# Kernel tuning notes

Measured on AMD Instinct MI355X. Metric: run time of the kernel, lower is better.

The kernel has to match this reference:

```python
import jax, jax.numpy as jnp
import numpy as np

LMAX, MMAX = 4, 2
L1 = LMAX + 1                      # 5 coefficients with m=0
NL = [LMAX + 1 - m for m in range(MMAX + 1)]   # [5,4,3] degrees per |m|
K = (LMAX + 1) ** 2                # 25 full SH coefficients
KR = NL[0] + 2 * sum(NL[1:])       # 19 coefficients with |m|<=mmax
# degree l of each row in the reduced (m-primary) layout:
# m=0: l=0..4 | m=+1: l=1..4 | m=-1: l=1..4 | m=+2: l=2..4 | m=-2: l=2..4
L_IDX = np.array([0,1,2,3,4, 1,2,3,4, 1,2,3,4, 2,3,4, 2,3,4])


def so2_conv(x, rad, w0, b0, wr1, wi1, wr2, wi2, c_out, extra):
    """SO(2)-equivariant conv over m-primary layout x: [E, KR, c_in].
    rad: optional per-edge radial weights [E, sum_m nl_m*c_in]."""
    E, _, c_in = x.shape
    # m = 0 block
    x0 = x[:, :L1].reshape(E, L1 * c_in)
    if rad is not None:
        x0 = x0 * rad[:, :L1 * c_in]
    y0 = x0 @ w0 + b0
    out0 = y0[:, :L1 * c_out].reshape(E, L1, c_out)
    gating = y0[:, L1 * c_out:] if extra else None
    outs = [out0]
    off_x, off_r = L1, L1 * c_in
    for nl, wr, wi in ((NL[1], wr1, wi1), (NL[2], wr2, wi2)):
        xr = x[:, off_x:off_x + nl].reshape(E, nl * c_in)
        xi = x[:, off_x + nl:off_x + 2 * nl].reshape(E, nl * c_in)
        if rad is not None:
            rm = rad[:, off_r:off_r + nl * c_in]
            xr, xi = xr * rm, xi * rm
        yr = xr @ wr - xi @ wi   # complex-style SO2 mixing
        yi = xi @ wr + xr @ wi
        outs += [yr.reshape(E, nl, c_out), yi.reshape(E, nl, c_out)]
        off_x += 2 * nl
        off_r += nl * c_in
    return jnp.concatenate(outs, axis=1), gating


def gate_act(gating, x):
    """GateActivation: silu on l=0 scalars, sigmoid gates per degree l>=1."""
    E, _, H = x.shape
    g = jax.nn.sigmoid(gating).reshape(E, LMAX, H)
    g_ext = jnp.concatenate([jnp.ones((E, 1, H), x.dtype), g], axis=1)
    out = x * g_ext[:, L_IDX]           # l=0 row gated by 1, replaced below
    return out.at[:, 0].set(jax.nn.silu(x[:, 0]))


def setup_inputs() -> dict:
    key = jax.random.key(0)
    ks = jax.random.split(key, 32)
    E, N, C, H, D, RH = 50000, 2500, 64, 64, 128, 64
    c_in1 = 2 * C
    rad_dim = sum(nl * c_in1 for nl in NL)          # 1536
    extra = LMAX * H                                 # 256

    def w(k, shape):
        return jax.random.normal(k, shape, jnp.float32) / np.sqrt(shape[0])

    inp = {
        'node_feats': jax.random.normal(ks[0], (N, K, C), jnp.float32),
        'edge_embeds': jax.random.normal(ks[1], (E, D), jnp.float32),
        'wigner': jax.random.normal(ks[2], (E, KR, K), jnp.float32) / np.sqrt(K),
        'wigner_inv': jax.random.normal(ks[3], (E, K, KR), jnp.float32) / np.sqrt(KR),
        'edge_envelope': jax.random.uniform(ks[4], (E, 1, 1), jnp.float32),
        'rad_w1': w(ks[5], (D, RH)), 'rad_b1': jnp.zeros((RH,), jnp.float32),
        'rad_w2': w(ks[6], (RH, rad_dim)), 'rad_b2': jnp.zeros((rad_dim,), jnp.float32),
        'w1_m0': w(ks[7], (L1 * c_in1, L1 * H + extra)),
        'b1_m0': jnp.zeros((L1 * H + extra,), jnp.float32),
        'w1_r1': w(ks[8], (NL[1] * c_in1, NL[1] * H)),
        'w1_i1': w(ks[9], (NL[1] * c_in1, NL[1] * H)),
        'w1_r2': w(ks[10], (NL[2] * c_in1, NL[2] * H)),
        'w1_i2': w(ks[11], (NL[2] * c_in1, NL[2] * H)),
        'w2_m0': w(ks[12], (L1 * H, L1 * C)),
        'b2_m0': jnp.zeros((L1 * C,), jnp.float32),
        'w2_r1': w(ks[13], (NL[1] * H, NL[1] * C)),
        'w2_i1': w(ks[14], (NL[1] * H, NL[1] * C)),
        'w2_r2': w(ks[15], (NL[2] * H, NL[2] * C)),
        'w2_i2': w(ks[16], (NL[2] * H, NL[2] * C)),
        'senders': jax.random.randint(ks[17], (E,), 0, N, jnp.int32),
        'receivers': jax.random.randint(ks[18], (E,), 0, N, jnp.int32),
    }
    return inp


def reference(node_feats, edge_embeds, wigner, wigner_inv, edge_envelope,
              rad_w1, rad_b1, rad_w2, rad_b2,
              w1_m0, b1_m0, w1_r1, w1_i1, w1_r2, w1_i2,
              w2_m0, b2_m0, w2_r1, w2_i1, w2_r2, w2_i2,
              senders, receivers):
    num_nodes = node_feats.shape[0]
    C = node_feats.shape[2]
    H = w2_m0.shape[0] // L1
    # gather + concat: [E, K, 2C]
    msg = jnp.concatenate((node_feats[senders], node_feats[receivers]), axis=2)
    # rotate to edge frame, truncated to |m|<=mmax: [E, KR, 2C]
    msg = jnp.einsum('erk,ekc->erc', wigner, msg)
    # per-edge radial weights for conv1
    rad = jax.nn.silu(edge_embeds @ rad_w1 + rad_b1) @ rad_w2 + rad_b2
    msg, gating = so2_conv(msg, rad, w1_m0, b1_m0, w1_r1, w1_i1, w1_r2, w1_i2,
                           c_out=H, extra=LMAX * H)
    msg = gate_act(gating, msg)
    msg, _ = so2_conv(msg, None, w2_m0, b2_m0, w2_r1, w2_i1, w2_r2, w2_i2,
                      c_out=C, extra=0)
    msg = msg * edge_envelope
    # rotate back to global frame: [E, K, C]
    msg = jnp.einsum('ekr,erc->ekc', wigner_inv, msg)
    return jax.ops.segment_sum(msg, receivers, num_segments=num_nodes)
```

## Files before the change

kernel.cpp:

```cpp
#include <hip/hip_runtime.h>


typedef __attribute__((ext_vector_type(8))) short bf16x8;
typedef __attribute__((ext_vector_type(4))) float f32x4;

union U8 { uint4 v; unsigned short s[8]; };

__device__ __forceinline__ unsigned short f2b(float f) {
    unsigned u = __float_as_uint(f);
    unsigned r = (u + 0x7FFFu + ((u >> 16) & 1u)) >> 16;
    return (unsigned short)r;
}
__device__ __forceinline__ float b2f(unsigned short h) {
    return __uint_as_float(((unsigned)h) << 16);
}
__device__ __forceinline__ float sigm_(float x){ return 1.0f/(1.0f+__expf(-x)); }
__device__ __forceinline__ float silu_(float x){ return x/(1.0f+__expf(-x)); }

__device__ __forceinline__ void async16(short* lds, const short* g) {
    __builtin_amdgcn_global_load_lds(
        (const __attribute__((address_space(1))) void*)g,
        (__attribute__((address_space(3))) void*)lds, 16, 0, 0);
}

#define OFF_W1T   0L
#define OFF_W1C1  409600L
#define OFF_W1C2  933888L
#define OFF_V0T   1327104L
#define OFF_V1C   1449984L
#define OFF_V2C   1712128L
#define OFF_RW2T  1908736L
#define W_TOTAL   2007040L
#define NNODES    2500
#define NFT_ELEMS (2500L * 2048L)

__global__ void k_prep(const float* __restrict__ w1m0, const float* __restrict__ w1r1,
                       const float* __restrict__ w1i1, const float* __restrict__ w1r2,
                       const float* __restrict__ w1i2, const float* __restrict__ w2m0,
                       const float* __restrict__ w2r1, const float* __restrict__ w2i1,
                       const float* __restrict__ w2r2, const float* __restrict__ w2i2,
                       const float* __restrict__ rw2, short* __restrict__ W)
{
    long i = (long)blockIdx.x * blockDim.x + threadIdx.x;
    if (i >= W_TOTAL) return;
    float v;
    if (i < OFF_W1C1) {
        int n = (int)(i / 640), k = (int)(i % 640);
        v = (n < 576) ? w1m0[k * 576 + n] : 0.f;
    } else if (i < OFF_W1C2) {
        long j = i - OFF_W1C1; int n = (int)(j >> 10), k = (int)(j & 1023);
        v = (n < 256) ? ((k < 512) ? w1r1[k*256 + n] : -w1i1[(k-512)*256 + n])
                      : ((k < 512) ? w1i1[k*256 + (n-256)] : w1r1[(k-512)*256 + (n-256)]);
    } else if (i < OFF_V0T) {
        long j = i - OFF_W1C2; int n = (int)(j / 768), k = (int)(j % 768);
        v = (n >= 384) ? 0.f
          : (n < 192) ? ((k < 384) ? w1r2[k*192 + n] : -w1i2[(k-384)*192 + n])
                      : ((k < 384) ? w1i2[k*192 + (n-192)] : w1r2[(k-384)*192 + (n-192)]);
    } else if (i < OFF_V1C) {
        long j = i - OFF_V0T; int n = (int)(j / 320), k = (int)(j % 320);
        v = (n < 320) ? w2m0[k * 320 + n] : 0.f;
    } else if (i < OFF_V2C) {
        long j = i - OFF_V1C; int n = (int)(j >> 9), k = (int)(j & 511);
        v = (n < 256) ? ((k < 256) ? w2r1[k*256 + n] : -w2i1[(k-256)*256 + n])
                      : ((k < 256) ? w2i1[k*256 + (n-256)] : w2r1[(k-256)*256 + (n-256)]);
    } else if (i < OFF_RW2T) {
        long j = i - OFF_V2C; int n = (int)(j / 384), k = (int)(j % 384);
        v = (n >= 384) ? 0.f
          : (n < 192) ? ((k < 192) ? w2r2[k*192 + n] : -w2i2[(k-192)*192 + n])
                      : ((k < 192) ? w2i2[k*192 + (n-192)] : w2r2[(k-192)*192 + (n-192)]);
    } else {
        long j = i - OFF_RW2T; int n = (int)(j >> 6), d = (int)(j & 63);
        v = rw2[d * 1536 + n];
    }
    W[i] = (short)f2b(v);
}

__global__ __launch_bounds__(256)
void k_nft(const float* __restrict__ nf, short* __restrict__ nfT)
{
    __shared__ float s_nf[25 * 65];
    const int t = threadIdx.x;
    const long nn = blockIdx.x;
    for (int p = t; p < 1600; p += 256) {
        int r = p >> 6, c = p & 63;
        s_nf[r * 65 + c] = nf[nn * 1600 + p];
    }
    __syncthreads();
    for (int i = t; i < 2048; i += 256) {
        int c = i >> 5, k = i & 31;
        float v = (k < 25) ? s_nf[k * 65 + c] : 0.f;
        nfT[nn * 2048 + i] = (short)f2b(v);
    }
}

__global__ void k_hist(const int* __restrict__ rcv, int* __restrict__ cnt, long e0, long n)
{
    long e = (long)blockIdx.x * 256 + threadIdx.x;
    if (e < n) atomicAdd(&cnt[rcv[e0 + e]], 1);
}

__global__ __launch_bounds__(256)
void k_scan(const int* __restrict__ cnt, int* __restrict__ off, int* __restrict__ nxt)
{
    __shared__ int part[256];
    const int t = threadIdx.x;
    const int base = t * 10;
    int loc[10]; int s = 0;
    #pragma unroll
    for (int j = 0; j < 10; ++j) {
        int idx = base + j;
        int v = (idx < NNODES) ? cnt[idx] : 0;
        loc[j] = s; s += v;
    }
    part[t] = s;
    __syncthreads();
    for (int d = 1; d < 256; d <<= 1) {
        int v = part[t];
        int u = (t >= d) ? part[t - d] : 0;
        __syncthreads();
        part[t] = v + u;
        __syncthreads();
    }
    int excl = (t == 0) ? 0 : part[t - 1];
    #pragma unroll
    for (int j = 0; j < 10; ++j) {
        int idx = base + j;
        if (idx < NNODES) { int o = excl + loc[j]; off[idx] = o; nxt[idx] = o; }
    }
}

__global__ void k_scat(const int* __restrict__ rcv, int* __restrict__ nxt,
                       int* __restrict__ perm, long e0, long n)
{
    long e = (long)blockIdx.x * 256 + threadIdx.x;
    if (e < n) {
        int p = atomicAdd(&nxt[rcv[e0 + e]], 1);
        perm[p] = (int)e;
    }
}

__global__ __launch_bounds__(512)
void k_rad(const float* __restrict__ ee, const float* __restrict__ rw1,
           const float* __restrict__ rb1, const float* __restrict__ rb2,
           const short* __restrict__ RW2T, short* __restrict__ rad,
           long e0, long Etot)
{
    __shared__ __align__(16) short s_h[32 * 64];
    const int t = threadIdx.x, w = t >> 6, l = t & 63, l15 = l & 15, lhi = l >> 4;
    const long eb = (long)blockIdx.x * 32;

    #pragma unroll
    for (int j = 0; j < 4; ++j) {
        int i = t + j * 512;
        int e = i >> 6, d = i & 63;
        long ge = e0 + eb + e;
        float a = rb1[d];
        if (ge < Etot) {
            const float* ep = ee + ge * 128;
            #pragma unroll 16
            for (int dd = 0; dd < 128; ++dd) a = fmaf(ep[dd], rw1[dd * 64 + d], a);
            a = silu_(a);
        } else a = 0.f;
        *(short*)((char*)s_h + e * 128 + ((d * 2) ^ ((e & 7) << 4))) = (short)f2b(a);
    }
    __syncthreads();

    f32x4 acc[6][2][2];
    #pragma unroll
    for (int g = 0; g < 6; ++g)
        #pragma unroll
        for (int mt = 0; mt < 2; ++mt)
            #pragma unroll
            for (int nt = 0; nt < 2; ++nt)
                acc[g][mt][nt] = (f32x4){0.f, 0.f, 0.f, 0.f};

    #pragma unroll
    for (int ks = 0; ks < 2; ++ks) {
        bf16x8 af[2];
        #pragma unroll
        for (int mt = 0; mt < 2; ++mt)
            af[mt] = *(const bf16x8*)((const char*)s_h + (mt * 16 + l15) * 128 +
                                      (((ks << 6) + (lhi << 4)) ^ ((l & 7) << 4)));
        #pragma unroll
        for (int g = 0; g < 6; ++g) {
            int grp = w + g * 8;
            #pragma unroll
            for (int nt = 0; nt < 2; ++nt) {
                int col = grp * 32 + nt * 16 + l15;
                bf16x8 bf = *(const bf16x8*)(RW2T + (long)col * 64 + (ks << 5) + (lhi << 3));
                #pragma unroll
                for (int mt = 0; mt < 2; ++mt)
                    acc[g][mt][nt] = __builtin_amdgcn_mfma_f32_16x16x32_bf16(af[mt], bf, acc[g][mt][nt], 0, 0, 0);
            }
        }
    }
    #pragma unroll
    for (int g = 0; g < 6; ++g)
        #pragma unroll
        for (int nt = 0; nt < 2; ++nt) {
            int col = (w + g * 8) * 32 + nt * 16 + l15;
            float bias = rb2[col];
            #pragma unroll
            for (int mt = 0; mt < 2; ++mt)
                #pragma unroll
                for (int r = 0; r < 4; ++r) {
                    int e = mt * 16 + lhi * 4 + r;
                    rad[(eb + e) * 1536 + col] = (short)f2b(acc[g][mt][nt][r] + bias);
                }
        }
}

__global__ __launch_bounds__(256)
void k_rot2(const float* __restrict__ wig, const short* __restrict__ nfT,
            const short* __restrict__ rad,
            const int* __restrict__ snd, const int* __restrict__ rcv,
            short* __restrict__ X, long e0, long nchunk)
{
    __shared__ float s_wg[4][480];
    __shared__ __align__(16) short s_rot[4][20 * 128];
    const int t = threadIdx.x, w = t >> 6, l = t & 63, l15 = l & 15, lhi = l >> 4;
    const long eb = (long)blockIdx.x * 4;
    const long el = eb + w;
    const bool valid = (el < nchunk);

    for (int p = t; p < 4 * 475; p += 256) {
        int e = p / 475, q = p - e * 475;
        if (eb + e < nchunk) s_wg[e][q] = wig[(e0 + eb + e) * 475 + q];
    }
    __syncthreads();

    if (valid) {
        long ge = e0 + el;
        int n0 = snd[ge], n1 = rcv[ge];
        U8 a0u, a1u;
        #pragma unroll
        for (int j = 0; j < 8; ++j) {
            int k = lhi * 8 + j;
            a0u.s[j] = (k < 25) ? f2b(s_wg[w][l15 * 25 + k]) : (unsigned short)0;
            a1u.s[j] = (l15 < 3 && k < 25) ? f2b(s_wg[w][(16 + l15) * 25 + k]) : (unsigned short)0;
        }
        bf16x8 a0 = *(bf16x8*)&a0u, a1 = *(bf16x8*)&a1u;

        f32x4 acc0[8], acc1[8];
        #pragma unroll
        for (int nt = 0; nt < 8; ++nt) {
            acc0[nt] = (f32x4){0.f, 0.f, 0.f, 0.f};
            acc1[nt] = (f32x4){0.f, 0.f, 0.f, 0.f};
        }
        #pragma unroll
        for (int nt = 0; nt < 8; ++nt) {
            int col = nt * 16 + l15;
            bf16x8 b = *(const bf16x8*)(nfT + (long)(col < 64 ? n0 : n1) * 2048 +
                                        (long)(col & 63) * 32 + (lhi << 3));
            acc0[nt] = __builtin_amdgcn_mfma_f32_16x16x32_bf16(a0, b, acc0[nt], 0, 0, 0);
            acc1[nt] = __builtin_amdgcn_mfma_f32_16x16x32_bf16(a1, b, acc1[nt], 0, 0, 0);
        }
        char* base = (char*)s_rot[w];
        #pragma unroll
        for (int nt = 0; nt < 8; ++nt) {
            int col2 = (nt * 16 + l15) * 2;
            #pragma unroll
            for (int r = 0; r < 4; ++r) {
                int row = lhi * 4 + r;
                *(short*)(base + ((row * 256 + col2) ^ ((row & 7) << 4))) = (short)f2b(acc0[nt][r]);
            }
            if (lhi == 0) {
                #pragma unroll
                for (int r = 0; r < 4; ++r) {
                    int row = 16 + r;
                    *(short*)(base + ((row * 256 + col2) ^ ((row & 7) << 4))) = (short)f2b(acc1[nt][r]);
                }
            }
        }
    }
    __syncthreads();

    short* xp = X + el * 2432;
    if (valid) {
        const short* rp = rad + el * 1536;
        #pragma unroll
        for (int it = 0; it < 5; ++it) {
            int q = l + it * 64;
            if (q < 304) {
                int r = q >> 4, c0 = (q & 15) << 3;
                int rr = (r < 9) ? r : ((r < 16) ? r - 4 : r - 7);
                U8 rot; rot.v = *(uint4*)((char*)s_rot[w] + ((r * 256 + c0 * 2) ^ ((r & 7) << 4)));
                U8 rd;  rd.v  = *(const uint4*)(rp + rr * 128 + c0);
                U8 o;
                #pragma unroll
                for (int j = 0; j < 8; ++j) o.s[j] = f2b(b2f(rot.s[j]) * b2f(rd.s[j]));
                *(uint4*)(xp + q * 8) = o.v;
            }
        }
    } else {
        #pragma unroll
        for (int it = 0; it < 5; ++it) {
            int q = l + it * 64;
            if (q < 304) *(uint4*)(xp + q * 8) = (uint4){0, 0, 0, 0};
        }
    }
}

__global__ __launch_bounds__(256)
void k_gate(short* __restrict__ Zr, long nitems)
{
    long idx = (long)blockIdx.x * 256 + threadIdx.x;
    if (idx >= nitems) return;
    long e = idx / 152;
    int jg = (int)(idx - e * 152);
    int j = jg * 8;
    short* rp = Zr + e * 1536;
    U8 z; z.v = *(const uint4*)(rp + j);
    U8 o;
    if (j < 320) {
        int rr = j >> 6;
        if (rr == 0) {
            #pragma unroll
            for (int q = 0; q < 8; ++q) o.s[q] = f2b(silu_(b2f(z.s[q])));
        } else {
            U8 g; g.v = *(const uint4*)(rp + 1216 + (rr - 1) * 64 + (j & 63));
            #pragma unroll
            for (int q = 0; q < 8; ++q) o.s[q] = f2b(b2f(z.s[q]) * b2f(g.s[q]));
        }
    } else if (j < 832) {
        U8 g; g.v = *(const uint4*)(rp + 1216 + ((j - 320) & 255));
        #pragma unroll
        for (int q = 0; q < 8; ++q) o.s[q] = f2b(b2f(z.s[q]) * b2f(g.s[q]));
    } else {
        int gi = j - 832; if (gi >= 192) gi -= 192;
        U8 g; g.v = *(const uint4*)(rp + 1280 + gi);
        #pragma unroll
        for (int q = 0; q < 8; ++q) o.s[q] = f2b(b2f(z.s[q]) * b2f(g.s[q]));
    }
    *(uint4*)(rp + j) = o.v;
}

template<int Km, int Nreal, int NBR, int EPI>
__device__ __forceinline__ void gemm_body(
    const short* __restrict__ A, const long RS,
    const short* __restrict__ W, const float* __restrict__ bias,
    short* __restrict__ O, const long OS, const int oofs,
    short* __restrict__ sA, short* __restrict__ sB, const int et, const int cb)
{
    const int t = threadIdx.x, w = t >> 6, l = t & 63, l15 = l & 15, lhi = l >> 4;
    const int wm = w & 1, wn = w >> 1;
    const long eb = (long)et * 128;
    const short* Ap = A + eb * RS;
    const short* Wp = W + (long)cb * Km;

    f32x4 acc[4][4];
    #pragma unroll
    for (int mt = 0; mt < 4; ++mt)
        #pragma unroll
        for (int nt = 0; nt < 4; ++nt)
            acc[mt][nt] = (f32x4){0.f, 0.f, 0.f, 0.f};

    int rowA[2], k8A[2];
    #pragma unroll
    for (int i = 0; i < 2; ++i) {
        int s = i * 512 + t;
        rowA[i] = s >> 3;
        k8A[i]  = (s & 7) ^ (rowA[i] & 7);
    }
    int rowB[4], k8B[4];
    #pragma unroll
    for (int i = 0; i < 4; ++i) {
        int s = i * 512 + t;
        rowB[i] = s >> 3;
        k8B[i]  = (s & 7) ^ (rowB[i] & 7);
    }
    const int wb = w << 6;

    const int rx = l & 7;
    constexpr int NCH = Km / 64;
    for (int ch = 0; ch < NCH; ++ch) {
        const int kc = ch * 64;
        __syncthreads();
        #pragma unroll
        for (int i = 0; i < 2; ++i)
            async16(sA + (i * 512 + wb) * 8, Ap + (long)rowA[i] * RS + kc + k8A[i] * 8);
        #pragma unroll
        for (int i = 0; i < 4; ++i) {
            if constexpr (NBR < 4) {
                if (rowB[i] < NBR * 64)
                    async16(sB + (i * 512 + wb) * 8, Wp + (long)rowB[i] * Km + kc + k8B[i] * 8);
            } else {
                async16(sB + (i * 512 + wb) * 8, Wp + (long)rowB[i] * Km + kc + k8B[i] * 8);
            }
        }
        __syncthreads();
        if (wn < NBR) {
            #pragma unroll
            for (int ks = 0; ks < 2; ++ks) {
                const int ko = (((ks << 2) + lhi) ^ rx) << 3;
                bf16x8 af[4], bf[4];
                #pragma unroll
                for (int mt = 0; mt < 4; ++mt) {
                    int row = wm * 64 + mt * 16 + l15;
                    af[mt] = *(const bf16x8*)(sA + row * 64 + ko);
                }
                #pragma unroll
                for (int nt = 0; nt < 4; ++nt) {
                    int row = wn * 64 + nt * 16 + l15;
                    bf[nt] = *(const bf16x8*)(sB + row * 64 + ko);
                }
                #pragma unroll
                for (int mt = 0; mt < 4; ++mt)
                    #pragma unroll
                    for (int nt = 0; nt < 4; ++nt)
                        acc[mt][nt] = __builtin_amdgcn_mfma_f32_16x16x32_bf16(af[mt], bf[nt], acc[mt][nt], 0, 0, 0);
            }
        }
    }

    if (wn >= NBR) return;
    const int r0 = wm * 64, c0 = wn * 64;
    #pragma unroll
    for (int nt = 0; nt < 4; ++nt) {
        int jj = cb + c0 + nt * 16 + l15;
        if (jj < Nreal) {
            float b = (EPI >= 1) ? bias[jj] : 0.f;
            #pragma unroll
            for (int mt = 0; mt < 4; ++mt)
                #pragma unroll
                for (int r = 0; r < 4; ++r) {
                    long e = eb + r0 + mt * 16 + lhi * 4 + r;
                    float v = acc[mt][nt][r] + b;
                    if constexpr (EPI == 2) {
                        if (jj < 320) O[e * OS + jj] = (short)f2b(v);
                        else          O[e * OS + 1216 + (jj - 320)] = (short)f2b(sigm_(v));
                    } else {
                        O[e * OS + oofs + jj] = (short)f2b(v);
                    }
                }
        }
    }
}

__global__ __launch_bounds__(512)
void k_conv1(const short* __restrict__ X, const short* __restrict__ W0,
             const short* __restrict__ W1, const short* __restrict__ W2,
             const float* __restrict__ b1m0, short* __restrict__ Zr, int nbt)
{
    __shared__ __align__(16) short sA[8192];
    __shared__ __align__(16) short sB[16384];
    const int bid = blockIdx.x;
    const int s = bid >> 3;
    const int et = (bid & 7) + ((s / 7) << 3);
    const int ph = s % 7;
    if (et >= nbt) return;
    if (ph < 2)
        gemm_body< 640, 576, 4, 2>(X,        2432, W0, b1m0,   Zr, 1536, 0,   sA, sB, et, ph << 8);
    else if (ph == 2)
        gemm_body< 640, 576, 1, 2>(X,        2432, W0, b1m0,   Zr, 1536, 0,   sA, sB, et, 2 << 8);
    else if (ph < 5)
        gemm_body<1024, 512, 4, 0>(X + 640,  2432, W1, nullptr, Zr, 1536, 320, sA, sB, et, (ph - 3) << 8);
    else if (ph == 5)
        gemm_body< 768, 384, 4, 0>(X + 1664, 2432, W2, nullptr, Zr, 1536, 832, sA, sB, et, 0);
    else
        gemm_body< 768, 384, 2, 0>(X + 1664, 2432, W2, nullptr, Zr, 1536, 832, sA, sB, et, 256);
}

__global__ __launch_bounds__(512)
void k_conv2(const short* __restrict__ Zr, const short* __restrict__ V0,
             const short* __restrict__ V1, const short* __restrict__ V2,
             const float* __restrict__ b2m0, short* __restrict__ Y2, int nbt)
{
    __shared__ __align__(16) short sA[8192];
    __shared__ __align__(16) short sB[16384];
    const int bid = blockIdx.x;
    const int s = bid >> 3;
    const int et = (bid & 7) + ((s / 6) << 3);
    const int ph = s % 6;
    if (et >= nbt) return;
    if (ph == 0)
        gemm_body<320, 320, 4, 1>(Zr,       1536, V0, b2m0,   Y2, 1216, 0,   sA, sB, et, 0);
    else if (ph == 1)
        gemm_body<320, 320, 1, 1>(Zr,       1536, V0, b2m0,   Y2, 1216, 0,   sA, sB, et, 256);
    else if (ph < 4)
        gemm_body<512, 512, 4, 0>(Zr + 320, 1536, V1, nullptr, Y2, 1216, 320, sA, sB, et, (ph - 2) << 8);
    else if (ph == 4)
        gemm_body<384, 384, 4, 0>(Zr + 832, 1536, V2, nullptr, Y2, 1216, 832, sA, sB, et, 0);
    else
        gemm_body<384, 384, 2, 0>(Zr + 832, 1536, V2, nullptr, Y2, 1216, 832, sA, sB, et, 256);
}

__global__ __launch_bounds__(256)
void k_invn(const short* __restrict__ Y2, const float* __restrict__ winv,
            const float* __restrict__ env, const int* __restrict__ cnt,
            const int* __restrict__ off, const int* __restrict__ perm,
            float* __restrict__ out, long e0)
{
    __shared__ __align__(16) short s_y[2][1216];
    __shared__ float s_wv[2][476];
    const int t = threadIdx.x;
    const int n = blockIdx.x;
    const int deg = cnt[n], start = off[n];

    float acc[7];
    #pragma unroll
    for (int j = 0; j < 7; ++j) acc[j] = 0.f;

    auto stage = [&](int i, int b) {
        int el = perm[start + i];
        long ge = e0 + el;
        if (t < 152) ((uint4*)s_y[b])[t] = *(const uint4*)(Y2 + (long)el * 1216 + t * 8);
        for (int p = t; p < 475; p += 256) s_wv[b][p] = winv[ge * 475 + p];
        if (t == 0) s_wv[b][475] = env[ge];
    };

    if (deg > 0) stage(0, 0);
    for (int i = 0; i < deg; ++i) {
        __syncthreads();
        if (i + 1 < deg) stage(i + 1, (i + 1) & 1);
        const short* sy = s_y[i & 1];
        const float* sw = s_wv[i & 1];
        float ev = sw[475];
        #pragma unroll
        for (int j = 0; j < 7; ++j) {
            int f = t + j * 256;
            if (f < 1600) {
                int r = f >> 6, c = f & 63;
                float a = 0.f;
                #pragma unroll
                for (int k = 0; k < 19; ++k)
                    a = fmaf(sw[r * 19 + k], b2f((unsigned short)sy[k * 64 + c]), a);
                acc[j] = fmaf(a, ev, acc[j]);
            }
        }
    }
    #pragma unroll
    for (int j = 0; j < 7; ++j) {
        int f = t + j * 256;
        if (f < 1600) out[(long)n * 1600 + f] += acc[j];
    }
}

extern "C" void kernel_launch(void* const* d_in, const int* in_sizes, int n_in,
                              void* d_out, int out_size, void* d_ws, size_t ws_size,
                              hipStream_t stream)
{
    const float* nf   = (const float*)d_in[0];
    const float* ee   = (const float*)d_in[1];
    const float* wig  = (const float*)d_in[2];
    const float* winv = (const float*)d_in[3];
    const float* env  = (const float*)d_in[4];
    const float* rw1  = (const float*)d_in[5];
    const float* rb1  = (const float*)d_in[6];
    const float* rw2  = (const float*)d_in[7];
    const float* rb2  = (const float*)d_in[8];
    const float* w1m0 = (const float*)d_in[9];
    const float* b1m0 = (const float*)d_in[10];
    const float* w1r1 = (const float*)d_in[11];
    const float* w1i1 = (const float*)d_in[12];
    const float* w1r2 = (const float*)d_in[13];
    const float* w1i2 = (const float*)d_in[14];
    const float* w2m0 = (const float*)d_in[15];
    const float* b2m0 = (const float*)d_in[16];
    const float* w2r1 = (const float*)d_in[17];
    const float* w2i1 = (const float*)d_in[18];
    const float* w2r2 = (const float*)d_in[19];
    const float* w2i2 = (const float*)d_in[20];
    const int*   snd  = (const int*)d_in[21];
    const int*   rcv  = (const int*)d_in[22];
    float* out = (float*)d_out;

    const long E = in_sizes[21];

    short* Wb  = (short*)d_ws;
    short* nfT = Wb + W_TOTAL;
    int* cnt   = (int*)(nfT + NFT_ELEMS);
    int* off   = cnt + 2512;
    int* nxt   = off + 2512;
    int* perm  = nxt + 2512;

    const size_t fixed = (size_t)W_TOTAL * 2 + (size_t)NFT_ELEMS * 2 + 3 * 2512 * 4;
    long cap = (ws_size > fixed) ? (long)((ws_size - fixed) / 7940) : 128;
    long chunk = (cap / 128) * 128;
    if (chunk < 128) chunk = 128;
    long Epad = ((E + 127) / 128) * 128;
    if (chunk > Epad) chunk = Epad;

    short* Xc = (short*)(perm + chunk);
    short* Rc = Xc + chunk * 2432;

    hipMemsetAsync(d_out, 0, (size_t)out_size * sizeof(float), stream);
    k_prep<<<(int)((W_TOTAL + 511) / 512), 512, 0, stream>>>(
        w1m0, w1r1, w1i1, w1r2, w1i2, w2m0, w2r1, w2i1, w2r2, w2i2, rw2, Wb);
    k_nft<<<NNODES, 256, 0, stream>>>(nf, nfT);

    for (long base = 0; base < E; base += chunk) {
        long n = E - base; if (n > chunk) n = chunk;
        int nb2 = (int)((n + 127) / 128);
        int nb8 = ((nb2 + 7) / 8) * 8;
        int nbe = (int)((n + 255) / 256);

        hipMemsetAsync(cnt, 0, NNODES * sizeof(int), stream);
        k_hist<<<nbe, 256, 0, stream>>>(rcv, cnt, base, n);
        k_scan<<<1, 256, 0, stream>>>(cnt, off, nxt);
        k_scat<<<nbe, 256, 0, stream>>>(rcv, nxt, perm, base, n);

        k_rad <<<(int)((n + 31) / 32), 512, 0, stream>>>(ee, rw1, rb1, rb2, Wb + OFF_RW2T, Rc, base, E);
        k_rot2<<<nb2 * 32, 256, 0, stream>>>(wig, nfT, Rc, snd, rcv, Xc, base, n);

        k_conv1<<<nb8 * 7, 512, 0, stream>>>(Xc, Wb + OFF_W1T, Wb + OFF_W1C1, Wb + OFF_W1C2, b1m0, Rc, nb2);

        long nitems = (long)nb2 * 128 * 152;
        k_gate<<<(int)((nitems + 255) / 256), 256, 0, stream>>>(Rc, nitems);

        k_conv2<<<nb8 * 6, 512, 0, stream>>>(Rc, Wb + OFF_V0T, Wb + OFF_V1C, Wb + OFF_V2C, b2m0, Xc, nb2);

        k_invn<<<NNODES, 256, 0, stream>>>(Xc, winv, env, cnt, off, perm, out, base);
    }
    (void)n_in;
}
```

Baseline: 1.041 ms.

## Fuse gate activation into conv2 GEMM A-operand loads

Removes the standalone k_gate kernel and applies the silu/sigmoid-gate multiply while conv2 loads its A tiles, through a new GMODE template parameter. The A operand now goes global→registers→LDS with the next chunk prefetched into registers, replacing the async global-to-LDS loads. This drops one full read-modify-write pass over the E×1536 intermediate. In exchange, gate vectors are re-read by every column block and the A path loses direct-to-LDS async loads.

```diff
diff --git a/kernel.cpp b/kernel.cpp
--- a/kernel.cpp
+++ b/kernel.cpp
@@ -301,43 +301,9 @@
     }
 }
 
-__global__ __launch_bounds__(256)
-void k_gate(short* __restrict__ Zr, long nitems)
-{
-    long idx = (long)blockIdx.x * 256 + threadIdx.x;
-    if (idx >= nitems) return;
-    long e = idx / 152;
-    int jg = (int)(idx - e * 152);
-    int j = jg * 8;
-    short* rp = Zr + e * 1536;
-    U8 z; z.v = *(const uint4*)(rp + j);
-    U8 o;
-    if (j < 320) {
-        int rr = j >> 6;
-        if (rr == 0) {
-            #pragma unroll
-            for (int q = 0; q < 8; ++q) o.s[q] = f2b(silu_(b2f(z.s[q])));
-        } else {
-            U8 g; g.v = *(const uint4*)(rp + 1216 + (rr - 1) * 64 + (j & 63));
-            #pragma unroll
-            for (int q = 0; q < 8; ++q) o.s[q] = f2b(b2f(z.s[q]) * b2f(g.s[q]));
-        }
-    } else if (j < 832) {
-        U8 g; g.v = *(const uint4*)(rp + 1216 + ((j - 320) & 255));
-        #pragma unroll
-        for (int q = 0; q < 8; ++q) o.s[q] = f2b(b2f(z.s[q]) * b2f(g.s[q]));
-    } else {
-        int gi = j - 832; if (gi >= 192) gi -= 192;
-        U8 g; g.v = *(const uint4*)(rp + 1280 + gi);
-        #pragma unroll
-        for (int q = 0; q < 8; ++q) o.s[q] = f2b(b2f(z.s[q]) * b2f(g.s[q]));
-    }
-    *(uint4*)(rp + j) = o.v;
-}
-
-template<int Km, int Nreal, int NBR, int EPI>
+template<int Km, int Nreal, int NBR, int GMODE, int EPI>
 __device__ __forceinline__ void gemm_body(
-    const short* __restrict__ A, const long RS,
+    const short* __restrict__ A, const long RS, const int gofs,
     const short* __restrict__ W, const float* __restrict__ bias,
     short* __restrict__ O, const long OS, const int oofs,
     short* __restrict__ sA, short* __restrict__ sB, const int et, const int cb)
@@ -371,14 +337,55 @@
     }
     const int wb = w << 6;
 
+    auto ldA = [&](int i, int kc) -> uint4 {
+        const short* rp = Ap + (long)rowA[i] * RS;
+        const int kg = kc + k8A[i] * 8;
+        uint4 z = *(const uint4*)(rp + kg);
+        if constexpr (GMODE == 0) return z;
+        U8 zz; zz.v = z; U8 r;
+        if constexpr (GMODE == 1) {
+            int rr = kg >> 6;
+            if (rr == 0) {
+                #pragma unroll
+                for (int q = 0; q < 8; ++q) r.s[q] = f2b(silu_(b2f(zz.s[q])));
+            } else {
+                U8 gg; gg.v = *(const uint4*)(rp + gofs + (rr - 1) * 64 + (kg & 63));
+                #pragma unroll
+                for (int q = 0; q < 8; ++q) r.s[q] = f2b(b2f(zz.s[q]) * b2f(gg.s[q]));
+            }
+        } else if constexpr (GMODE == 2) {
+            U8 gg; gg.v = *(const uint4*)(rp + gofs + (kg & 255));
+            #pragma unroll
+            for (int q = 0; q < 8; ++q) r.s[q] = f2b(b2f(zz.s[q]) * b2f(gg.s[q]));
+        } else {
+            int gi = 64 + kg - ((kg >= 192) ? 192 : 0);
+            U8 gg; gg.v = *(const uint4*)(rp + gofs + gi);
+            #pragma unroll
+            for (int q = 0; q < 8; ++q) r.s[q] = f2b(b2f(zz.s[q]) * b2f(gg.s[q]));
+        }
+        return r.v;
+    };
+
+    uint4 rAv[2];
+    if constexpr (GMODE != 0) {
+        rAv[0] = ldA(0, 0);
+        rAv[1] = ldA(1, 0);
+    }
+
     const int rx = l & 7;
     constexpr int NCH = Km / 64;
     for (int ch = 0; ch < NCH; ++ch) {
         const int kc = ch * 64;
         __syncthreads();
-        #pragma unroll
-        for (int i = 0; i < 2; ++i)
-            async16(sA + (i * 512 + wb) * 8, Ap + (long)rowA[i] * RS + kc + k8A[i] * 8);
+        if constexpr (GMODE == 0) {
+            #pragma unroll
+            for (int i = 0; i < 2; ++i)
+                async16(sA + (i * 512 + wb) * 8, Ap + (long)rowA[i] * RS + kc + k8A[i] * 8);
+        } else {
+            #pragma unroll
+            for (int i = 0; i < 2; ++i)
+                *(uint4*)(sA + (i * 512 + t) * 8) = rAv[i];
+        }
         #pragma unroll
         for (int i = 0; i < 4; ++i) {
             if constexpr (NBR < 4) {
@@ -386,6 +393,12 @@
                     async16(sB + (i * 512 + wb) * 8, Wp + (long)rowB[i] * Km + kc + k8B[i] * 8);
             } else {
                 async16(sB + (i * 512 + wb) * 8, Wp + (long)rowB[i] * Km + kc + k8B[i] * 8);
+            }
+        }
+        if constexpr (GMODE != 0) {
+            if (ch + 1 < NCH) {
+                rAv[0] = ldA(0, kc + 64);
+                rAv[1] = ldA(1, kc + 64);
             }
         }
         __syncthreads();
@@ -450,15 +463,15 @@
     const int ph = s % 7;
     if (et >= nbt) return;
     if (ph < 2)
-        gemm_body< 640, 576, 4, 2>(X,        2432, W0, b1m0,   Zr, 1536, 0,   sA, sB, et, ph << 8);
+        gemm_body< 640, 576, 4, 0, 2>(X,        2432, 0, W0, b1m0,   Zr, 1536, 0,   sA, sB, et, ph << 8);
     else if (ph == 2)
-        gemm_body< 640, 576, 1, 2>(X,        2432, W0, b1m0,   Zr, 1536, 0,   sA, sB, et, 2 << 8);
+        gemm_body< 640, 576, 1, 0, 2>(X,        2432, 0, W0, b1m0,   Zr, 1536, 0,   sA, sB, et, 2 << 8);
     else if (ph < 5)
-        gemm_body<1024, 512, 4, 0>(X + 640,  2432, W1, nullptr, Zr, 1536, 320, sA, sB, et, (ph - 3) << 8);
+        gemm_body<1024, 512, 4, 0, 0>(X + 640,  2432, 0, W1, nullptr, Zr, 1536, 320, sA, sB, et, (ph - 3) << 8);
     else if (ph == 5)
-        gemm_body< 768, 384, 4, 0>(X + 1664, 2432, W2, nullptr, Zr, 1536, 832, sA, sB, et, 0);
+        gemm_body< 768, 384, 4, 0, 0>(X + 1664, 2432, 0, W2, nullptr, Zr, 1536, 832, sA, sB, et, 0);
     else
-        gemm_body< 768, 384, 2, 0>(X + 1664, 2432, W2, nullptr, Zr, 1536, 832, sA, sB, et, 256);
+        gemm_body< 768, 384, 2, 0, 0>(X + 1664, 2432, 0, W2, nullptr, Zr, 1536, 832, sA, sB, et, 256);
 }
 
 __global__ __launch_bounds__(512)
@@ -474,15 +487,15 @@
     const int ph = s % 6;
     if (et >= nbt) return;
     if (ph == 0)
-        gemm_body<320, 320, 4, 1>(Zr,       1536, V0, b2m0,   Y2, 1216, 0,   sA, sB, et, 0);
+        gemm_body<320, 320, 4, 1, 1>(Zr,       1536, 1216, V0, b2m0,   Y2, 1216, 0,   sA, sB, et, 0);
     else if (ph == 1)
-        gemm_body<320, 320, 1, 1>(Zr,       1536, V0, b2m0,   Y2, 1216, 0,   sA, sB, et, 256);
+        gemm_body<320, 320, 1, 1, 1>(Zr,       1536, 1216, V0, b2m0,   Y2, 1216, 0,   sA, sB, et, 256);
     else if (ph < 4)
-        gemm_body<512, 512, 4, 0>(Zr + 320, 1536, V1, nullptr, Y2, 1216, 320, sA, sB, et, (ph - 2) << 8);
+        gemm_body<512, 512, 4, 2, 0>(Zr + 320, 1536, 896,  V1, nullptr, Y2, 1216, 320, sA, sB, et, (ph - 2) << 8);
     else if (ph == 4)
-        gemm_body<384, 384, 4, 0>(Zr + 832, 1536, V2, nullptr, Y2, 1216, 832, sA, sB, et, 0);
+        gemm_body<384, 384, 4, 3, 0>(Zr + 832, 1536, 384,  V2, nullptr, Y2, 1216, 832, sA, sB, et, 0);
     else
-        gemm_body<384, 384, 2, 0>(Zr + 832, 1536, V2, nullptr, Y2, 1216, 832, sA, sB, et, 256);
+        gemm_body<384, 384, 2, 3, 0>(Zr + 832, 1536, 384,  V2, nullptr, Y2, 1216, 832, sA, sB, et, 256);
 }
 
 __global__ __launch_bounds__(256)
@@ -604,10 +617,6 @@
         k_rot2<<<nb2 * 32, 256, 0, stream>>>(wig, nfT, Rc, snd, rcv, Xc, base, n);
 
         k_conv1<<<nb8 * 7, 512, 0, stream>>>(Xc, Wb + OFF_W1T, Wb + OFF_W1C1, Wb + OFF_W1C2, b1m0, Rc, nb2);
-
-        long nitems = (long)nb2 * 128 * 152;
-        k_gate<<<(int)((nitems + 255) / 256), 256, 0, stream>>>(Rc, nitems);
-
         k_conv2<<<nb8 * 6, 512, 0, stream>>>(Rc, Wb + OFF_V0T, Wb + OFF_V1C, Wb + OFF_V2C, b2m0, Xc, nb2);
 
         k_invn<<<NNODES, 256, 0, stream>>>(Xc, winv, env, cnt, off, perm, out, base);
```

After: 1.035 ms. About the same (-0.6%).
